# Optimization experiments

Measured on AMD Instinct MI355X. Metric: run time of the kernel, lower is better.

The kernel has to match this reference:

```python
import jax, jax.numpy as jnp
import numpy as np

N = 50000          # nodes (ogbn-products-like subgraph)
E = 800000         # directed edges (avg degree 16)
F_IN, HID, HEADS, OUT = 100, 32, 4, 47
W1 = HID * HEADS   # 128
NEG_SLOPE = 0.2
BN_EPS = 1e-5


def _gatv2(x, src, dst, w_src, w_dst, att, bias, heads, ch):
    """GATv2Conv (PyG semantics, share_weights=False, concat).
    x: [N, F]; src/dst: [Etot] (self-loops already appended);
    w_src/w_dst: [F, heads*ch]; att: [heads, ch]; bias: [heads*ch].
    """
    n = x.shape[0]
    xl = (x @ w_src).reshape(n, heads, ch)   # source-side transform
    xr = (x @ w_dst).reshape(n, heads, ch)   # target-side transform
    # per-edge attention logits: a . leaky_relu(xl[j] + xr[i])  -> [E, heads]
    e = jnp.sum(jax.nn.leaky_relu(xl[src] + xr[dst], NEG_SLOPE) * att, axis=-1)
    # segment softmax over incoming edges of each destination node
    m = jax.ops.segment_max(e, dst, num_segments=n)          # [N, heads]
    ex = jnp.exp(e - m[dst])
    denom = jax.ops.segment_sum(ex, dst, num_segments=n)     # [N, heads]
    alpha = ex / denom[dst]                                  # [E, heads]
    # weighted scatter-add aggregation of source features
    out = jax.ops.segment_sum(alpha[:, :, None] * xl[src], dst, num_segments=n)
    return out.reshape(n, heads * ch) + bias


def _bn_eval(x, g, b, m, v):
    return (x - m) * jax.lax.rsqrt(v + BN_EPS) * g + b


def setup_inputs() -> dict:
    key = jax.random.key(0)
    ks = jax.random.split(key, 32)
    s = 0.1
    inp = {
        "x": jax.random.normal(ks[0], (N, F_IN), jnp.float32),
        "edge_index": jax.random.randint(ks[1], (2, E), 0, N, dtype=jnp.int32),
        "w1_src": jax.random.normal(ks[2], (F_IN, W1), jnp.float32) * s,
        "w1_dst": jax.random.normal(ks[3], (F_IN, W1), jnp.float32) * s,
        "att1": jax.random.normal(ks[4], (HEADS, HID), jnp.float32) * s,
        "b1": jnp.zeros((W1,), jnp.float32),
        "bn1_g": jnp.ones((W1,), jnp.float32),
        "bn1_b": jnp.zeros((W1,), jnp.float32),
        "bn1_m": jax.random.normal(ks[5], (W1,), jnp.float32) * 0.05,
        "bn1_v": jax.random.uniform(ks[6], (W1,), jnp.float32, 0.5, 1.5),
        "res0_w": jax.random.normal(ks[7], (F_IN, W1), jnp.float32) * s,
        "res0_b": jnp.zeros((W1,), jnp.float32),
        "w2_src": jax.random.normal(ks[8], (W1, W1), jnp.float32) * s,
        "w2_dst": jax.random.normal(ks[9], (W1, W1), jnp.float32) * s,
        "att2": jax.random.normal(ks[10], (HEADS, HID), jnp.float32) * s,
        "b2": jnp.zeros((W1,), jnp.float32),
        "bn2_g": jnp.ones((W1,), jnp.float32),
        "bn2_b": jnp.zeros((W1,), jnp.float32),
        "bn2_m": jax.random.normal(ks[11], (W1,), jnp.float32) * 0.05,
        "bn2_v": jax.random.uniform(ks[12], (W1,), jnp.float32, 0.5, 1.5),
        # layer 3: 128 -> 47, heads=1
        "w3_src": jax.random.normal(ks[13], (W1, OUT), jnp.float32) * s,
        "w3_dst": jax.random.normal(ks[14], (W1, OUT), jnp.float32) * s,
        "att3": jax.random.normal(ks[15], (1, OUT), jnp.float32) * s,
        "b3": jnp.zeros((OUT,), jnp.float32),
        "bn3_g": jnp.ones((OUT,), jnp.float32),
        "bn3_b": jnp.zeros((OUT,), jnp.float32),
        "bn3_m": jax.random.normal(ks[16], (OUT,), jnp.float32) * 0.05,
        "bn3_v": jax.random.uniform(ks[17], (OUT,), jnp.float32, 0.5, 1.5),
        "res2_w": jax.random.normal(ks[18], (W1, OUT), jnp.float32) * s,
        "res2_b": jnp.zeros((OUT,), jnp.float32),
    }
    return inp


def reference(x, edge_index,
              w1_src, w1_dst, att1, b1, bn1_g, bn1_b, bn1_m, bn1_v, res0_w, res0_b,
              w2_src, w2_dst, att2, b2, bn2_g, bn2_b, bn2_m, bn2_v,
              w3_src, w3_dst, att3, b3, bn3_g, bn3_b, bn3_m, bn3_v, res2_w, res2_b):
    # add self-loops (PyG GATv2Conv default add_self_loops=True)
    loops = jnp.arange(x.shape[0], dtype=edge_index.dtype)
    src = jnp.concatenate([edge_index[0], loops])
    dst = jnp.concatenate([edge_index[1], loops])

    # layer 1 + linear residual + BN + relu (eval mode: no dropout)
    h = _gatv2(x, src, dst, w1_src, w1_dst, att1, b1, HEADS, HID)
    h = h + (x @ res0_w + res0_b)
    h = jax.nn.relu(_bn_eval(h, bn1_g, bn1_b, bn1_m, bn1_v))

    # layer 2 + identity residual + BN + relu
    h2 = _gatv2(h, src, dst, w2_src, w2_dst, att2, b2, HEADS, HID)
    h2 = h2 + h
    h2 = jax.nn.relu(_bn_eval(h2, bn2_g, bn2_b, bn2_m, bn2_v))

    # layer 3 (heads=1) + linear residual + BN (no relu/dropout on last layer)
    out = _gatv2(h2, src, dst, w3_src, w3_dst, att3, b3, 1, OUT)
    out = out + (h2 @ res2_w + res2_b)
    out = _bn_eval(out, bn3_g, bn3_b, bn3_m, bn3_v)
    return out
```

## Files before the change

kernel.cpp:

```cpp
#include <hip/hip_runtime.h>
#include <math.h>

#define BN_EPS 1e-5f
#define SLOT 96
#define LN16 2.7725887f

typedef _Float16 h2 __attribute__((ext_vector_type(2)));
typedef _Float16 h8 __attribute__((ext_vector_type(8)));
typedef float f2v __attribute__((ext_vector_type(2)));
typedef float float4v __attribute__((ext_vector_type(4)));

static __device__ inline h2 bit_h2(unsigned u) {
    union { unsigned u; h2 h; } c; c.u = u; return c.h;
}
static __device__ inline unsigned bit_u(h2 h) {
    union { unsigned u; h2 h; } c; c.h = h; return c.u;
}

template <int CTRL>
static __device__ inline float dpp_add(float x) {
    int y = __builtin_amdgcn_update_dpp(0, __float_as_int(x), CTRL, 0xF, 0xF, true);
    return x + __int_as_float(y);
}
static __device__ inline float red8_dpp(float t) {
    t = dpp_add<0xB1>(t); t = dpp_add<0x4E>(t); t = dpp_add<0x141>(t);
    return t;
}
static __device__ inline float red16_dpp(float t) {
    t = dpp_add<0xB1>(t); t = dpp_add<0x4E>(t); t = dpp_add<0x141>(t);
    t = dpp_add<0x140>(t);
    return t;
}

static __device__ inline void pack_one(int idx,
                                       const float* p0, const float* p1,
                                       const float* p2,
                                       int w0, int w1, int w2,
                                       int Ksrc, int Ncat,
                                       _Float16* out) {
    int k = idx / Ncat, n = idx - k * Ncat;
    float v = 0.f;
    if (k < Ksrc) {
        if (n < w0) v = p0[(size_t)k * w0 + n];
        else if (n < w0 + w1) v = p1[(size_t)k * w1 + (n - w0)];
        else if (w2 > 0 && n < w0 + w1 + w2) v = p2[(size_t)k * w2 + (n - w0 - w1)];
    }
    int kt = k >> 5, kr = k & 31;
    int quad = kr >> 3, j = kr & 7;
    int nt = n >> 4, nr = n & 15;
    int ntiles = Ncat >> 4;
    out[((size_t)(kt * ntiles + nt) * 64 + quad * 16 + nr) * 8 + j] = (_Float16)v;
}

__global__ __launch_bounds__(256) void prep_scat_k(
    const int* __restrict__ src, const int* __restrict__ dst, int E, int Etot,
    int* __restrict__ cnt, int* __restrict__ esrc, int scatBlocks,
    const float* __restrict__ x, _Float16* __restrict__ A, int N,
    const float* __restrict__ w1s, const float* __restrict__ w1d,
    const float* __restrict__ r0w, const float* __restrict__ w2s,
    const float* __restrict__ w2d, const float* __restrict__ w3s,
    const float* __restrict__ w3d, const float* __restrict__ r2w,
    _Float16* __restrict__ Wb1, _Float16* __restrict__ Wb2,
    _Float16* __restrict__ Wb3) {
    if ((int)blockIdx.x < scatBlocks) {
        int i = blockIdx.x * 256 + threadIdx.x;
        if (i < Etot) {
            int d = (i < E) ? dst[i] : (i - E);
            int s = (i < E) ? src[i] : (i - E);
            int pos = atomicAdd(&cnt[d], 1);
            esrc[(size_t)d * SLOT + pos] = s << 9;
        }
        return;
    }
    const int S1 = 128 * 384, S2 = 128 * 256, S3 = 128 * 144;
    int convTot = N * 128;
    int idx = (blockIdx.x - scatBlocks) * 256 + threadIdx.x;
    if (idx < convTot) {
        int n = idx >> 7, k = idx & 127;
        A[idx] = (_Float16)(k < 100 ? x[(size_t)n * 100 + k] : 0.f);
        return;
    }
    int p = idx - convTot;
    if (p < S1) pack_one(p, w1s, w1d, r0w, 128, 128, 128, 100, 384, Wb1);
    else if (p < S1 + S2) pack_one(p - S1, w2s, w2d, nullptr, 128, 128, 0, 128, 256, Wb2);
    else if (p < S1 + S2 + S3) pack_one(p - S1 - S2, w3s, w3d, r2w, 47, 47, 47, 128, 144, Wb3);
}

template <int NT>
__global__ __launch_bounds__(256) void mfma_gemm(const _Float16* __restrict__ A,
                                                 const _Float16* __restrict__ Bp,
                                                 _Float16* __restrict__ XLR,
                                                 float* __restrict__ RES,
                                                 int M, int Kpad, int Ncat,
                                                 int ncat_valid, int res_off,
                                                 int bf_remap, int bf_shift,
                                                 int bf_stride, int res_stride) {
    int wid = (blockIdx.x * 256 + threadIdx.x) >> 6;
    int lane = threadIdx.x & 63;
    int ngroups = Ncat / (16 * NT);
    int mtiles = M >> 4;
    int mt = wid / ngroups;
    int ng = wid - mt * ngroups;
    if (mt >= mtiles) return;
    int quad = lane >> 4;
    int nr = lane & 15;
    int row = mt * 16 + nr;
    int ntiles = Ncat >> 4;

    float4v acc[NT];
#pragma unroll
    for (int t = 0; t < NT; t++) acc[t] = (float4v){0.f, 0.f, 0.f, 0.f};

    for (int k0 = 0; k0 < Kpad; k0 += 32) {
        h8 a = *(const h8*)(A + (size_t)row * Kpad + k0 + quad * 8);
        int kt = k0 >> 5;
        const _Float16* bbase =
            Bp + ((size_t)(kt * ntiles + ng * NT) * 64 + lane) * 8;
#pragma unroll
        for (int t = 0; t < NT; t++) {
            h8 b = *(const h8*)(bbase + (size_t)t * 64 * 8);
            acc[t] = __builtin_amdgcn_mfma_f32_16x16x32_f16(a, b, acc[t], 0, 0, 0);
        }
    }
    int rowb = mt * 16 + quad * 4;
#pragma unroll
    for (int t = 0; t < NT; t++) {
        int col = (ng * NT + t) * 16 + nr;
        if (col >= ncat_valid) continue;
        if (col < res_off) {
            int bc = (col >= bf_remap) ? col + bf_shift : col;
#pragma unroll
            for (int r = 0; r < 4; r++)
                XLR[(size_t)(rowb + r) * bf_stride + bc] = (_Float16)acc[t][r];
        } else {
            int rc = col - res_off;
#pragma unroll
            for (int r = 0; r < 4; r++)
                RES[(size_t)(rowb + r) * res_stride + rc] = acc[t][r];
        }
    }
}

__global__ __launch_bounds__(256) void gat_agg4_fused(
    const int* __restrict__ cnt, const int* __restrict__ esrc,
    const _Float16* __restrict__ xlr, const float* __restrict__ att,
    const float* __restrict__ RES, const float* __restrict__ resB,
    const float* __restrict__ bias,
    const float* __restrict__ g, const float* __restrict__ bb,
    const float* __restrict__ mm, const float* __restrict__ vv,
    _Float16* __restrict__ hbf, int N, int mode) {
    int d = blockIdx.x * 4 + (threadIdx.x >> 6);
    if (d >= N) return;
    int lane = threadIdx.x & 63;
    int half = lane >> 5;
    int gl = lane & 31;
    int c0 = gl * 4;
    const char* xb = (const char*)xlr + c0 * 2;
    const h2 NS = {(_Float16)0.2f, (_Float16)0.2f};

    uint2 xrv = *(const uint2*)(xb + (size_t)d * 512 + 256);
    h2 xr01 = bit_h2(xrv.x), xr23 = bit_h2(xrv.y);
    float4 af = *(const float4*)(att + c0);
    h2 at01 = {(_Float16)af.x, (_Float16)af.y};
    h2 at23 = {(_Float16)af.z, (_Float16)af.w};

    int beg = d * SLOT;
    int end = beg + cnt[d];
    float den = 0.f;
    h2 acc01 = {(_Float16)0.f, (_Float16)0.f};
    h2 acc23 = acc01;
    int j = beg;
    for (; j + 4 <= end; j += 4) {
        int o0 = esrc[j + half];
        int o1 = esrc[j + 2 + half];
        uint2 u0 = *(const uint2*)(xb + o0);
        uint2 u1 = *(const uint2*)(xb + o1);
        h2 a01 = bit_h2(u0.x), a23 = bit_h2(u0.y);
        h2 b01 = bit_h2(u1.x), b23 = bit_h2(u1.y);
        h2 v01 = a01 + xr01, v23 = a23 + xr23;
        h2 w01 = b01 + xr01, w23 = b23 + xr23;
        v01 = __builtin_elementwise_max(v01, v01 * NS);
        v23 = __builtin_elementwise_max(v23, v23 * NS);
        w01 = __builtin_elementwise_max(w01, w01 * NS);
        w23 = __builtin_elementwise_max(w23, w23 * NS);
        h2 t2a = v01 * at01 + v23 * at23;
        h2 t2b = w01 * at01 + w23 * at23;
        f2v ta = __builtin_convertvector(t2a, f2v);
        f2v tb = __builtin_convertvector(t2b, f2v);
        float t0 = ta.x + ta.y;
        float t1 = tb.x + tb.y;
        t0 = red8_dpp(t0);
        t1 = red8_dpp(t1);
        float p0 = __expf(t0 - LN16);
        float p1 = __expf(t1 - LN16);
        den += p0 + p1;
        h2 P0 = {(_Float16)p0, (_Float16)p0};
        h2 P1 = {(_Float16)p1, (_Float16)p1};
        acc01 = P0 * a01 + acc01;
        acc23 = P0 * a23 + acc23;
        acc01 = P1 * b01 + acc01;
        acc23 = P1 * b23 + acc23;
    }
    for (; j < end; j += 2) {
        int jj = j + half;
        bool act = jj < end;
        int o = esrc[act ? jj : (end - 1)];
        uint2 u0 = *(const uint2*)(xb + o);
        h2 a01 = bit_h2(u0.x), a23 = bit_h2(u0.y);
        h2 v01 = a01 + xr01, v23 = a23 + xr23;
        v01 = __builtin_elementwise_max(v01, v01 * NS);
        v23 = __builtin_elementwise_max(v23, v23 * NS);
        h2 t2 = v01 * at01 + v23 * at23;
        f2v tf = __builtin_convertvector(t2, f2v);
        float t = tf.x + tf.y;
        t = red8_dpp(t);
        float p = act ? __expf(t - LN16) : 0.f;
        den += p;
        h2 P = {(_Float16)p, (_Float16)p};
        acc01 = P * a01 + acc01;
        acc23 = P * a23 + acc23;
    }
    den += __shfl_xor(den, 32);
    f2v c01 = __builtin_convertvector(acc01, f2v);
    f2v c23 = __builtin_convertvector(acc23, f2v);
    float f0 = c01.x, f1 = c01.y, fA = c23.x, fB = c23.y;
    f0 += __shfl_xor(f0, 32);
    f1 += __shfl_xor(f1, 32);
    fA += __shfl_xor(fA, 32);
    fB += __shfl_xor(fB, 32);

    if (half == 0) {
        float inv = 1.f / den;
        float4 bi = *(const float4*)(bias + c0);
        float o0 = f0 * inv + bi.x;
        float o1 = f1 * inv + bi.y;
        float o2 = fA * inv + bi.z;
        float o3 = fB * inv + bi.w;
        if (mode == 1) {
            float4 r = *(const float4*)(RES + (size_t)d * 128 + c0);
            float4 rb = *(const float4*)(resB + c0);
            o0 += r.x + rb.x; o1 += r.y + rb.y;
            o2 += r.z + rb.z; o3 += r.w + rb.w;
        } else {
            uint2 hv = *(const uint2*)(hbf + (size_t)d * 128 + c0);
            f2v g01 = __builtin_convertvector(bit_h2(hv.x), f2v);
            f2v g23 = __builtin_convertvector(bit_h2(hv.y), f2v);
            o0 += g01.x; o1 += g01.y; o2 += g23.x; o3 += g23.y;
        }
        float4 gm = *(const float4*)(mm + c0);
        float4 gv = *(const float4*)(vv + c0);
        float4 gg = *(const float4*)(g + c0);
        float4 gb = *(const float4*)(bb + c0);
        o0 = fmaxf((o0 - gm.x) * rsqrtf(gv.x + BN_EPS) * gg.x + gb.x, 0.f);
        o1 = fmaxf((o1 - gm.y) * rsqrtf(gv.y + BN_EPS) * gg.y + gb.y, 0.f);
        o2 = fmaxf((o2 - gm.z) * rsqrtf(gv.z + BN_EPS) * gg.z + gb.z, 0.f);
        o3 = fmaxf((o3 - gm.w) * rsqrtf(gv.w + BN_EPS) * gg.w + gb.w, 0.f);
        h2 s01 = {(_Float16)o0, (_Float16)o1};
        h2 s23 = {(_Float16)o2, (_Float16)o3};
        uint2 w;
        w.x = bit_u(s01);
        w.y = bit_u(s23);
        *(uint2*)(hbf + (size_t)d * 128 + c0) = w;
    }
}

__global__ __launch_bounds__(256) void gat_agg1_fused(
    const int* __restrict__ cnt, const int* __restrict__ esrc,
    const _Float16* __restrict__ xlr, const float* __restrict__ att,
    const float* __restrict__ RES, const float* __restrict__ resB,
    const float* __restrict__ bias,
    const float* __restrict__ g, const float* __restrict__ bb,
    const float* __restrict__ mm, const float* __restrict__ vv,
    float* __restrict__ out, int N) {
    int d = blockIdx.x * 4 + (threadIdx.x >> 6);
    if (d >= N) return;
    int lane = threadIdx.x & 63;
    int gl = lane & 15, grp = lane >> 4;
    const char* xb = (const char*)xlr + gl * 8;
    const h2 NS = {(_Float16)0.2f, (_Float16)0.2f};

    uint2 xrv = *(const uint2*)(xb + (size_t)d * 256 + 128);
    h2 xr01 = bit_h2(xrv.x), xr23 = bit_h2(xrv.y);
    float atf[4];
#pragma unroll
    for (int k = 0; k < 4; k++) {
        int c = gl * 4 + k;
        atf[k] = (c < 47) ? att[c] : 0.f;
    }
    h2 at01 = {(_Float16)atf[0], (_Float16)atf[1]};
    h2 at23 = {(_Float16)atf[2], (_Float16)atf[3]};

    int beg = d * SLOT;
    int end = beg + cnt[d];
    float den = 0.f;
    h2 acc01 = {(_Float16)0.f, (_Float16)0.f};
    h2 acc23 = acc01;
    int j = beg + grp;
    for (; j + 4 < end; j += 8) {
        int o0 = esrc[j] >> 1;
        int o1 = esrc[j + 4] >> 1;
        uint2 u0 = *(const uint2*)(xb + o0);
        uint2 u1 = *(const uint2*)(xb + o1);
        h2 a01 = bit_h2(u0.x), a23 = bit_h2(u0.y);
        h2 b01 = bit_h2(u1.x), b23 = bit_h2(u1.y);
        h2 v01 = a01 + xr01, v23 = a23 + xr23;
        h2 w01 = b01 + xr01, w23 = b23 + xr23;
        v01 = __builtin_elementwise_max(v01, v01 * NS);
        v23 = __builtin_elementwise_max(v23, v23 * NS);
        w01 = __builtin_elementwise_max(w01, w01 * NS);
        w23 = __builtin_elementwise_max(w23, w23 * NS);
        h2 t2a = v01 * at01 + v23 * at23;
        h2 t2b = w01 * at01 + w23 * at23;
        f2v ta = __builtin_convertvector(t2a, f2v);
        f2v tb = __builtin_convertvector(t2b, f2v);
        float t0 = ta.x + ta.y;
        float t1 = tb.x + tb.y;
        t0 = red16_dpp(t0);
        t1 = red16_dpp(t1);
        float p0 = __expf(t0 - LN16);
        float p1 = __expf(t1 - LN16);
        den += p0 + p1;
        h2 P0 = {(_Float16)p0, (_Float16)p0};
        h2 P1 = {(_Float16)p1, (_Float16)p1};
        acc01 = P0 * a01 + acc01;
        acc23 = P0 * a23 + acc23;
        acc01 = P1 * b01 + acc01;
        acc23 = P1 * b23 + acc23;
    }
    if (j < end) {
        int o = esrc[j] >> 1;
        uint2 u0 = *(const uint2*)(xb + o);
        h2 a01 = bit_h2(u0.x), a23 = bit_h2(u0.y);
        h2 v01 = a01 + xr01, v23 = a23 + xr23;
        v01 = __builtin_elementwise_max(v01, v01 * NS);
        v23 = __builtin_elementwise_max(v23, v23 * NS);
        h2 t2 = v01 * at01 + v23 * at23;
        f2v tf = __builtin_convertvector(t2, f2v);
        float t = tf.x + tf.y;
        t = red16_dpp(t);
        float p = __expf(t - LN16);
        den += p;
        h2 P = {(_Float16)p, (_Float16)p};
        acc01 = P * a01 + acc01;
        acc23 = P * a23 + acc23;
    }
    den += __shfl_xor(den, 16);
    den += __shfl_xor(den, 32);
    f2v c01 = __builtin_convertvector(acc01, f2v);
    f2v c23 = __builtin_convertvector(acc23, f2v);
    float f[4] = {c01.x, c01.y, c23.x, c23.y};
#pragma unroll
    for (int k = 0; k < 4; k++) {
        f[k] += __shfl_xor(f[k], 16);
        f[k] += __shfl_xor(f[k], 32);
    }
    if (grp == 0 && gl < 12) {
        float inv = 1.f / den;
#pragma unroll
        for (int k = 0; k < 4; k++) {
            int c = gl * 4 + k;
            if (c < 47) {
                float o = f[k] * inv + bias[c] + RES[(size_t)d * 48 + c] + resB[c];
                o = (o - mm[c]) * rsqrtf(vv[c] + BN_EPS) * g[c] + bb[c];
                out[(size_t)d * 47 + c] = o;
            }
        }
    }
}

extern "C" void kernel_launch(void* const* d_in, const int* in_sizes, int n_in,
                              void* d_out, int out_size, void* d_ws, size_t ws_size,
                              hipStream_t stream) {
    const float* x      = (const float*)d_in[0];
    const int*   ei     = (const int*)d_in[1];
    const float* w1_src = (const float*)d_in[2];
    const float* w1_dst = (const float*)d_in[3];
    const float* att1   = (const float*)d_in[4];
    const float* b1     = (const float*)d_in[5];
    const float* bn1_g  = (const float*)d_in[6];
    const float* bn1_b  = (const float*)d_in[7];
    const float* bn1_m  = (const float*)d_in[8];
    const float* bn1_v  = (const float*)d_in[9];
    const float* res0_w = (const float*)d_in[10];
    const float* res0_b = (const float*)d_in[11];
    const float* w2_src = (const float*)d_in[12];
    const float* w2_dst = (const float*)d_in[13];
    const float* att2   = (const float*)d_in[14];
    const float* b2     = (const float*)d_in[15];
    const float* bn2_g  = (const float*)d_in[16];
    const float* bn2_b  = (const float*)d_in[17];
    const float* bn2_m  = (const float*)d_in[18];
    const float* bn2_v  = (const float*)d_in[19];
    const float* w3_src = (const float*)d_in[20];
    const float* w3_dst = (const float*)d_in[21];
    const float* att3   = (const float*)d_in[22];
    const float* b3     = (const float*)d_in[23];
    const float* bn3_g  = (const float*)d_in[24];
    const float* bn3_b  = (const float*)d_in[25];
    const float* bn3_m  = (const float*)d_in[26];
    const float* bn3_v  = (const float*)d_in[27];
    const float* res2_w = (const float*)d_in[28];
    const float* res2_b = (const float*)d_in[29];

    const int F_IN = 100;
    const int KP = 128;
    const int NC1 = 384, NC2 = 256, NC3 = 144;
    int N = in_sizes[0] / F_IN;
    int E = in_sizes[1] / 2;
    int Etot = E + N;
    const int* src = ei;
    const int* dst = ei + E;

    float* ws = (float*)d_ws;
    size_t o = 0;
    _Float16* XLR = (_Float16*)(ws + o); o += (size_t)N * 128;
    float* B_res = ws + o; o += (size_t)N * 128;
    _Float16* A_h = (_Float16*)(ws + o); o += (size_t)N * 64;
    _Float16* Wb1 = (_Float16*)(ws + o); o += (size_t)KP * NC1 / 2;
    _Float16* Wb2 = (_Float16*)(ws + o); o += (size_t)KP * NC2 / 2;
    _Float16* Wb3 = (_Float16*)(ws + o); o += (size_t)KP * NC3 / 2;
    int* I_cnt  = (int*)(ws + o); o += N;
    int* I_esrc = (int*)(ws + o); o += (size_t)N * SLOT + 4;
    (void)ws_size; (void)n_in; (void)out_size;

    int mtiles = (N + 15) / 16;
    int aggGrid = (N + 3) / 4;

    hipMemsetAsync(I_cnt, 0, (size_t)N * sizeof(int), stream);

    {
        int sb = (Etot + 255) / 256;
        int prepTot = N * KP + KP * (NC1 + NC2 + NC3);
        int pb = (prepTot + 255) / 256;
        prep_scat_k<<<sb + pb, 256, 0, stream>>>(
            src, dst, E, Etot, I_cnt, I_esrc, sb, x, A_h, N,
            w1_src, w1_dst, res0_w, w2_src, w2_dst, w3_src, w3_dst, res2_w,
            Wb1, Wb2, Wb3);
    }

    {
        int waves = mtiles * (NC1 / 64);
        mfma_gemm<4><<<(waves + 3) / 4, 256, 0, stream>>>(
            A_h, Wb1, XLR, B_res, N, KP, NC1, 384, 256, 384, 0, 256, 128);
    }
    gat_agg4_fused<<<aggGrid, 256, 0, stream>>>(
        I_cnt, I_esrc, XLR, att1, B_res, res0_b, b1,
        bn1_g, bn1_b, bn1_m, bn1_v, A_h, N, 1);

    {
        int waves = mtiles * (NC2 / 64);
        mfma_gemm<4><<<(waves + 3) / 4, 256, 0, stream>>>(
            A_h, Wb2, XLR, B_res, N, KP, NC2, 256, 256, 256, 0, 256, 128);
    }
    gat_agg4_fused<<<aggGrid, 256, 0, stream>>>(
        I_cnt, I_esrc, XLR, att2, nullptr, nullptr, b2,
        bn2_g, bn2_b, bn2_m, bn2_v, A_h, N, 2);

    {
        int waves = mtiles * (NC3 / 48);
        mfma_gemm<3><<<(waves + 3) / 4, 256, 0, stream>>>(
            A_h, Wb3, XLR, B_res, N, KP, NC3, 141, 94, 47, 17, 128, 48);
    }
    gat_agg1_fused<<<aggGrid, 256, 0, stream>>>(
        I_cnt, I_esrc, XLR, att3, B_res, res2_b, b3,
        bn3_g, bn3_b, bn3_m, bn3_v, (float*)d_out, N);
}
```

Baseline: 394.4 us.

## Fuse all stages into one persistent cooperative kernel with grid syncs

Replaces the memset and seven separate kernel launches with a single cooperative persistent kernel. Stages are separated by grid.sync() and use grid-stride loops. The edge scatter now overlaps with the first GEMM, and per-thread BN constants are hoisted out of the node loop. The aim is to remove launch gaps and tail effects, at the cost of grid-wide barrier overhead and occupancy capped by the fused kernel's register use.

```diff
diff --git a/kernel.cpp b/kernel.cpp
--- a/kernel.cpp
+++ b/kernel.cpp
@@ -1,5 +1,8 @@
 #include <hip/hip_runtime.h>
+#include <hip/hip_cooperative_groups.h>
 #include <math.h>
+
+namespace cg = cooperative_groups;
 
 #define BN_EPS 1e-5f
 #define SLOT 96
@@ -31,6 +34,24 @@
     t = dpp_add<0x140>(t);
     return t;
 }
+
+struct P {
+    const int* src; const int* dst; int E; int Etot; int N;
+    const float* x;
+    const float* w1s; const float* w1d; const float* r0w; const float* r0b;
+    const float* att1; const float* b1;
+    const float* bn1g; const float* bn1b; const float* bn1m; const float* bn1v;
+    const float* w2s; const float* w2d;
+    const float* att2; const float* b2;
+    const float* bn2g; const float* bn2b; const float* bn2m; const float* bn2v;
+    const float* w3s; const float* w3d; const float* r2w; const float* r2b;
+    const float* att3; const float* b3;
+    const float* bn3g; const float* bn3b; const float* bn3m; const float* bn3v;
+    _Float16* XLR; float* RES; _Float16* A;
+    _Float16* Wb1; _Float16* Wb2; _Float16* Wb3;
+    int* cnt; int* esrc;
+    float* out;
+};
 
 static __device__ inline void pack_one(int idx,
                                        const float* p0, const float* p1,
@@ -52,364 +73,342 @@
     out[((size_t)(kt * ntiles + nt) * 64 + quad * 16 + nr) * 8 + j] = (_Float16)v;
 }
 
-__global__ __launch_bounds__(256) void prep_scat_k(
-    const int* __restrict__ src, const int* __restrict__ dst, int E, int Etot,
-    int* __restrict__ cnt, int* __restrict__ esrc, int scatBlocks,
-    const float* __restrict__ x, _Float16* __restrict__ A, int N,
-    const float* __restrict__ w1s, const float* __restrict__ w1d,
-    const float* __restrict__ r0w, const float* __restrict__ w2s,
-    const float* __restrict__ w2d, const float* __restrict__ w3s,
-    const float* __restrict__ w3d, const float* __restrict__ r2w,
-    _Float16* __restrict__ Wb1, _Float16* __restrict__ Wb2,
-    _Float16* __restrict__ Wb3) {
-    if ((int)blockIdx.x < scatBlocks) {
-        int i = blockIdx.x * 256 + threadIdx.x;
-        if (i < Etot) {
-            int d = (i < E) ? dst[i] : (i - E);
-            int s = (i < E) ? src[i] : (i - E);
-            int pos = atomicAdd(&cnt[d], 1);
-            esrc[(size_t)d * SLOT + pos] = s << 9;
-        }
-        return;
-    }
-    const int S1 = 128 * 384, S2 = 128 * 256, S3 = 128 * 144;
-    int convTot = N * 128;
-    int idx = (blockIdx.x - scatBlocks) * 256 + threadIdx.x;
-    if (idx < convTot) {
-        int n = idx >> 7, k = idx & 127;
-        A[idx] = (_Float16)(k < 100 ? x[(size_t)n * 100 + k] : 0.f);
-        return;
-    }
-    int p = idx - convTot;
-    if (p < S1) pack_one(p, w1s, w1d, r0w, 128, 128, 128, 100, 384, Wb1);
-    else if (p < S1 + S2) pack_one(p - S1, w2s, w2d, nullptr, 128, 128, 0, 128, 256, Wb2);
-    else if (p < S1 + S2 + S3) pack_one(p - S1 - S2, w3s, w3d, r2w, 47, 47, 47, 128, 144, Wb3);
-}
-
 template <int NT>
-__global__ __launch_bounds__(256) void mfma_gemm(const _Float16* __restrict__ A,
-                                                 const _Float16* __restrict__ Bp,
-                                                 _Float16* __restrict__ XLR,
-                                                 float* __restrict__ RES,
-                                                 int M, int Kpad, int Ncat,
-                                                 int ncat_valid, int res_off,
-                                                 int bf_remap, int bf_shift,
-                                                 int bf_stride, int res_stride) {
-    int wid = (blockIdx.x * 256 + threadIdx.x) >> 6;
+static __device__ void gemm_phase(const _Float16* __restrict__ A,
+                                  const _Float16* __restrict__ Bp,
+                                  _Float16* __restrict__ XLR,
+                                  float* __restrict__ RES,
+                                  int M, int Ncat, int ncat_valid, int res_off,
+                                  int bf_remap, int bf_shift,
+                                  int bf_stride, int res_stride) {
     int lane = threadIdx.x & 63;
+    int gw = blockIdx.x * 4 + (threadIdx.x >> 6);
+    int gws = gridDim.x * 4;
     int ngroups = Ncat / (16 * NT);
     int mtiles = M >> 4;
-    int mt = wid / ngroups;
-    int ng = wid - mt * ngroups;
-    if (mt >= mtiles) return;
+    int ntiles = Ncat >> 4;
     int quad = lane >> 4;
     int nr = lane & 15;
-    int row = mt * 16 + nr;
-    int ntiles = Ncat >> 4;
-
-    float4v acc[NT];
-#pragma unroll
-    for (int t = 0; t < NT; t++) acc[t] = (float4v){0.f, 0.f, 0.f, 0.f};
-
-    for (int k0 = 0; k0 < Kpad; k0 += 32) {
-        h8 a = *(const h8*)(A + (size_t)row * Kpad + k0 + quad * 8);
-        int kt = k0 >> 5;
-        const _Float16* bbase =
-            Bp + ((size_t)(kt * ntiles + ng * NT) * 64 + lane) * 8;
+    for (int w = gw; w < mtiles * ngroups; w += gws) {
+        int mt = w / ngroups;
+        int ng = w - mt * ngroups;
+        int row = mt * 16 + nr;
+        float4v acc[NT];
+#pragma unroll
+        for (int t = 0; t < NT; t++) acc[t] = (float4v){0.f, 0.f, 0.f, 0.f};
+#pragma unroll
+        for (int k0 = 0; k0 < 128; k0 += 32) {
+            h8 a = *(const h8*)(A + (size_t)row * 128 + k0 + quad * 8);
+            int kt = k0 >> 5;
+            const _Float16* bbase =
+                Bp + ((size_t)(kt * ntiles + ng * NT) * 64 + lane) * 8;
+#pragma unroll
+            for (int t = 0; t < NT; t++) {
+                h8 b = *(const h8*)(bbase + (size_t)t * 512);
+                acc[t] = __builtin_amdgcn_mfma_f32_16x16x32_f16(a, b, acc[t], 0, 0, 0);
+            }
+        }
+        int rowb = mt * 16 + quad * 4;
 #pragma unroll
         for (int t = 0; t < NT; t++) {
-            h8 b = *(const h8*)(bbase + (size_t)t * 64 * 8);
-            acc[t] = __builtin_amdgcn_mfma_f32_16x16x32_f16(a, b, acc[t], 0, 0, 0);
-        }
-    }
-    int rowb = mt * 16 + quad * 4;
-#pragma unroll
-    for (int t = 0; t < NT; t++) {
-        int col = (ng * NT + t) * 16 + nr;
-        if (col >= ncat_valid) continue;
-        if (col < res_off) {
-            int bc = (col >= bf_remap) ? col + bf_shift : col;
-#pragma unroll
-            for (int r = 0; r < 4; r++)
-                XLR[(size_t)(rowb + r) * bf_stride + bc] = (_Float16)acc[t][r];
-        } else {
-            int rc = col - res_off;
-#pragma unroll
-            for (int r = 0; r < 4; r++)
-                RES[(size_t)(rowb + r) * res_stride + rc] = acc[t][r];
-        }
-    }
-}
-
-__global__ __launch_bounds__(256) void gat_agg4_fused(
-    const int* __restrict__ cnt, const int* __restrict__ esrc,
-    const _Float16* __restrict__ xlr, const float* __restrict__ att,
-    const float* __restrict__ RES, const float* __restrict__ resB,
-    const float* __restrict__ bias,
-    const float* __restrict__ g, const float* __restrict__ bb,
-    const float* __restrict__ mm, const float* __restrict__ vv,
-    _Float16* __restrict__ hbf, int N, int mode) {
-    int d = blockIdx.x * 4 + (threadIdx.x >> 6);
-    if (d >= N) return;
+            int col = (ng * NT + t) * 16 + nr;
+            if (col >= ncat_valid) continue;
+            if (col < res_off) {
+                int bc = (col >= bf_remap) ? col + bf_shift : col;
+#pragma unroll
+                for (int r = 0; r < 4; r++)
+                    XLR[(size_t)(rowb + r) * bf_stride + bc] = (_Float16)acc[t][r];
+            } else {
+                int rc = col - res_off;
+#pragma unroll
+                for (int r = 0; r < 4; r++)
+                    RES[(size_t)(rowb + r) * res_stride + rc] = acc[t][r];
+            }
+        }
+    }
+}
+
+static __device__ void agg4_phase(const P& p, const float* __restrict__ att,
+                                  const float* __restrict__ RES,
+                                  const float* __restrict__ resB,
+                                  const float* __restrict__ bias,
+                                  const float* __restrict__ g,
+                                  const float* __restrict__ bb,
+                                  const float* __restrict__ mm,
+                                  const float* __restrict__ vv, int mode) {
+    int gw = blockIdx.x * 4 + (threadIdx.x >> 6);
+    int gws = gridDim.x * 4;
     int lane = threadIdx.x & 63;
     int half = lane >> 5;
     int gl = lane & 31;
     int c0 = gl * 4;
-    const char* xb = (const char*)xlr + c0 * 2;
+    const char* xb = (const char*)p.XLR + c0 * 2;
     const h2 NS = {(_Float16)0.2f, (_Float16)0.2f};
 
-    uint2 xrv = *(const uint2*)(xb + (size_t)d * 512 + 256);
-    h2 xr01 = bit_h2(xrv.x), xr23 = bit_h2(xrv.y);
     float4 af = *(const float4*)(att + c0);
     h2 at01 = {(_Float16)af.x, (_Float16)af.y};
     h2 at23 = {(_Float16)af.z, (_Float16)af.w};
-
-    int beg = d * SLOT;
-    int end = beg + cnt[d];
-    float den = 0.f;
-    h2 acc01 = {(_Float16)0.f, (_Float16)0.f};
-    h2 acc23 = acc01;
-    int j = beg;
-    for (; j + 4 <= end; j += 4) {
-        int o0 = esrc[j + half];
-        int o1 = esrc[j + 2 + half];
-        uint2 u0 = *(const uint2*)(xb + o0);
-        uint2 u1 = *(const uint2*)(xb + o1);
-        h2 a01 = bit_h2(u0.x), a23 = bit_h2(u0.y);
-        h2 b01 = bit_h2(u1.x), b23 = bit_h2(u1.y);
-        h2 v01 = a01 + xr01, v23 = a23 + xr23;
-        h2 w01 = b01 + xr01, w23 = b23 + xr23;
-        v01 = __builtin_elementwise_max(v01, v01 * NS);
-        v23 = __builtin_elementwise_max(v23, v23 * NS);
-        w01 = __builtin_elementwise_max(w01, w01 * NS);
-        w23 = __builtin_elementwise_max(w23, w23 * NS);
-        h2 t2a = v01 * at01 + v23 * at23;
-        h2 t2b = w01 * at01 + w23 * at23;
-        f2v ta = __builtin_convertvector(t2a, f2v);
-        f2v tb = __builtin_convertvector(t2b, f2v);
-        float t0 = ta.x + ta.y;
-        float t1 = tb.x + tb.y;
-        t0 = red8_dpp(t0);
-        t1 = red8_dpp(t1);
-        float p0 = __expf(t0 - LN16);
-        float p1 = __expf(t1 - LN16);
-        den += p0 + p1;
-        h2 P0 = {(_Float16)p0, (_Float16)p0};
-        h2 P1 = {(_Float16)p1, (_Float16)p1};
-        acc01 = P0 * a01 + acc01;
-        acc23 = P0 * a23 + acc23;
-        acc01 = P1 * b01 + acc01;
-        acc23 = P1 * b23 + acc23;
-    }
-    for (; j < end; j += 2) {
-        int jj = j + half;
-        bool act = jj < end;
-        int o = esrc[act ? jj : (end - 1)];
-        uint2 u0 = *(const uint2*)(xb + o);
-        h2 a01 = bit_h2(u0.x), a23 = bit_h2(u0.y);
-        h2 v01 = a01 + xr01, v23 = a23 + xr23;
-        v01 = __builtin_elementwise_max(v01, v01 * NS);
-        v23 = __builtin_elementwise_max(v23, v23 * NS);
-        h2 t2 = v01 * at01 + v23 * at23;
-        f2v tf = __builtin_convertvector(t2, f2v);
-        float t = tf.x + tf.y;
-        t = red8_dpp(t);
-        float p = act ? __expf(t - LN16) : 0.f;
-        den += p;
-        h2 P = {(_Float16)p, (_Float16)p};
-        acc01 = P * a01 + acc01;
-        acc23 = P * a23 + acc23;
-    }
-    den += __shfl_xor(den, 32);
-    f2v c01 = __builtin_convertvector(acc01, f2v);
-    f2v c23 = __builtin_convertvector(acc23, f2v);
-    float f0 = c01.x, f1 = c01.y, fA = c23.x, fB = c23.y;
-    f0 += __shfl_xor(f0, 32);
-    f1 += __shfl_xor(f1, 32);
-    fA += __shfl_xor(fA, 32);
-    fB += __shfl_xor(fB, 32);
-
-    if (half == 0) {
-        float inv = 1.f / den;
-        float4 bi = *(const float4*)(bias + c0);
-        float o0 = f0 * inv + bi.x;
-        float o1 = f1 * inv + bi.y;
-        float o2 = fA * inv + bi.z;
-        float o3 = fB * inv + bi.w;
-        if (mode == 1) {
-            float4 r = *(const float4*)(RES + (size_t)d * 128 + c0);
-            float4 rb = *(const float4*)(resB + c0);
-            o0 += r.x + rb.x; o1 += r.y + rb.y;
-            o2 += r.z + rb.z; o3 += r.w + rb.w;
-        } else {
-            uint2 hv = *(const uint2*)(hbf + (size_t)d * 128 + c0);
-            f2v g01 = __builtin_convertvector(bit_h2(hv.x), f2v);
-            f2v g23 = __builtin_convertvector(bit_h2(hv.y), f2v);
-            o0 += g01.x; o1 += g01.y; o2 += g23.x; o3 += g23.y;
-        }
-        float4 gm = *(const float4*)(mm + c0);
-        float4 gv = *(const float4*)(vv + c0);
-        float4 gg = *(const float4*)(g + c0);
-        float4 gb = *(const float4*)(bb + c0);
-        o0 = fmaxf((o0 - gm.x) * rsqrtf(gv.x + BN_EPS) * gg.x + gb.x, 0.f);
-        o1 = fmaxf((o1 - gm.y) * rsqrtf(gv.y + BN_EPS) * gg.y + gb.y, 0.f);
-        o2 = fmaxf((o2 - gm.z) * rsqrtf(gv.z + BN_EPS) * gg.z + gb.z, 0.f);
-        o3 = fmaxf((o3 - gm.w) * rsqrtf(gv.w + BN_EPS) * gg.w + gb.w, 0.f);
-        h2 s01 = {(_Float16)o0, (_Float16)o1};
-        h2 s23 = {(_Float16)o2, (_Float16)o3};
-        uint2 w;
-        w.x = bit_u(s01);
-        w.y = bit_u(s23);
-        *(uint2*)(hbf + (size_t)d * 128 + c0) = w;
-    }
-}
-
-__global__ __launch_bounds__(256) void gat_agg1_fused(
-    const int* __restrict__ cnt, const int* __restrict__ esrc,
-    const _Float16* __restrict__ xlr, const float* __restrict__ att,
-    const float* __restrict__ RES, const float* __restrict__ resB,
-    const float* __restrict__ bias,
-    const float* __restrict__ g, const float* __restrict__ bb,
-    const float* __restrict__ mm, const float* __restrict__ vv,
-    float* __restrict__ out, int N) {
-    int d = blockIdx.x * 4 + (threadIdx.x >> 6);
-    if (d >= N) return;
+    float4 bi = *(const float4*)(bias + c0);
+    float4 gm = *(const float4*)(mm + c0);
+    float4 gv = *(const float4*)(vv + c0);
+    float4 gg = *(const float4*)(g + c0);
+    float4 gb = *(const float4*)(bb + c0);
+    float4 rb = (mode == 1) ? *(const float4*)(resB + c0)
+                            : (float4){0.f, 0.f, 0.f, 0.f};
+    float rs0 = rsqrtf(gv.x + BN_EPS), rs1 = rsqrtf(gv.y + BN_EPS);
+    float rs2 = rsqrtf(gv.z + BN_EPS), rs3 = rsqrtf(gv.w + BN_EPS);
+
+    for (int d = gw; d < p.N; d += gws) {
+        uint2 xrv = *(const uint2*)(xb + (size_t)d * 512 + 256);
+        h2 xr01 = bit_h2(xrv.x), xr23 = bit_h2(xrv.y);
+        int beg = d * SLOT;
+        int end = beg + p.cnt[d];
+        float den = 0.f;
+        h2 acc01 = {(_Float16)0.f, (_Float16)0.f};
+        h2 acc23 = acc01;
+        int j = beg;
+        for (; j + 4 <= end; j += 4) {
+            int o0 = p.esrc[j + half];
+            int o1 = p.esrc[j + 2 + half];
+            uint2 u0 = *(const uint2*)(xb + o0);
+            uint2 u1 = *(const uint2*)(xb + o1);
+            h2 a01 = bit_h2(u0.x), a23 = bit_h2(u0.y);
+            h2 b01 = bit_h2(u1.x), b23 = bit_h2(u1.y);
+            h2 v01 = a01 + xr01, v23 = a23 + xr23;
+            h2 w01 = b01 + xr01, w23 = b23 + xr23;
+            v01 = __builtin_elementwise_max(v01, v01 * NS);
+            v23 = __builtin_elementwise_max(v23, v23 * NS);
+            w01 = __builtin_elementwise_max(w01, w01 * NS);
+            w23 = __builtin_elementwise_max(w23, w23 * NS);
+            h2 t2a = v01 * at01 + v23 * at23;
+            h2 t2b = w01 * at01 + w23 * at23;
+            f2v ta = __builtin_convertvector(t2a, f2v);
+            f2v tb = __builtin_convertvector(t2b, f2v);
+            float t0 = red8_dpp(ta.x + ta.y);
+            float t1 = red8_dpp(tb.x + tb.y);
+            float p0 = __expf(t0 - LN16);
+            float p1 = __expf(t1 - LN16);
+            den += p0 + p1;
+            h2 P0 = {(_Float16)p0, (_Float16)p0};
+            h2 P1 = {(_Float16)p1, (_Float16)p1};
+            acc01 = P0 * a01 + acc01;
+            acc23 = P0 * a23 + acc23;
+            acc01 = P1 * b01 + acc01;
+            acc23 = P1 * b23 + acc23;
+        }
+        for (; j < end; j += 2) {
+            int jj = j + half;
+            bool act = jj < end;
+            int o = p.esrc[act ? jj : (end - 1)];
+            uint2 u0 = *(const uint2*)(xb + o);
+            h2 a01 = bit_h2(u0.x), a23 = bit_h2(u0.y);
+            h2 v01 = a01 + xr01, v23 = a23 + xr23;
+            v01 = __builtin_elementwise_max(v01, v01 * NS);
+            v23 = __builtin_elementwise_max(v23, v23 * NS);
+            h2 t2 = v01 * at01 + v23 * at23;
+            f2v tf = __builtin_convertvector(t2, f2v);
+            float t = red8_dpp(tf.x + tf.y);
+            float pp = act ? __expf(t - LN16) : 0.f;
+            den += pp;
+            h2 PP = {(_Float16)pp, (_Float16)pp};
+            acc01 = PP * a01 + acc01;
+            acc23 = PP * a23 + acc23;
+        }
+        den += __shfl_xor(den, 32);
+        f2v c01 = __builtin_convertvector(acc01, f2v);
+        f2v c23 = __builtin_convertvector(acc23, f2v);
+        float f0 = c01.x, f1 = c01.y, fA = c23.x, fB = c23.y;
+        f0 += __shfl_xor(f0, 32);
+        f1 += __shfl_xor(f1, 32);
+        fA += __shfl_xor(fA, 32);
+        fB += __shfl_xor(fB, 32);
+
+        if (half == 0) {
+            float inv = 1.f / den;
+            float o0 = f0 * inv + bi.x;
+            float o1 = f1 * inv + bi.y;
+            float o2 = fA * inv + bi.z;
+            float o3 = fB * inv + bi.w;
+            if (mode == 1) {
+                float4 r = *(const float4*)(RES + (size_t)d * 128 + c0);
+                o0 += r.x + rb.x; o1 += r.y + rb.y;
+                o2 += r.z + rb.z; o3 += r.w + rb.w;
+            } else {
+                uint2 hv = *(const uint2*)(p.A + (size_t)d * 128 + c0);
+                f2v g01 = __builtin_convertvector(bit_h2(hv.x), f2v);
+                f2v g23 = __builtin_convertvector(bit_h2(hv.y), f2v);
+                o0 += g01.x; o1 += g01.y; o2 += g23.x; o3 += g23.y;
+            }
+            o0 = fmaxf((o0 - gm.x) * rs0 * gg.x + gb.x, 0.f);
+            o1 = fmaxf((o1 - gm.y) * rs1 * gg.y + gb.y, 0.f);
+            o2 = fmaxf((o2 - gm.z) * rs2 * gg.z + gb.z, 0.f);
+            o3 = fmaxf((o3 - gm.w) * rs3 * gg.w + gb.w, 0.f);
+            h2 s01 = {(_Float16)o0, (_Float16)o1};
+            h2 s23 = {(_Float16)o2, (_Float16)o3};
+            uint2 w;
+            w.x = bit_u(s01);
+            w.y = bit_u(s23);
+            *(uint2*)(p.A + (size_t)d * 128 + c0) = w;
+        }
+    }
+}
+
+static __device__ void agg1_phase(const P& p) {
+    int gw = blockIdx.x * 4 + (threadIdx.x >> 6);
+    int gws = gridDim.x * 4;
     int lane = threadIdx.x & 63;
     int gl = lane & 15, grp = lane >> 4;
-    const char* xb = (const char*)xlr + gl * 8;
+    const char* xb = (const char*)p.XLR + gl * 8;
     const h2 NS = {(_Float16)0.2f, (_Float16)0.2f};
 
-    uint2 xrv = *(const uint2*)(xb + (size_t)d * 256 + 128);
-    h2 xr01 = bit_h2(xrv.x), xr23 = bit_h2(xrv.y);
     float atf[4];
 #pragma unroll
     for (int k = 0; k < 4; k++) {
         int c = gl * 4 + k;
-        atf[k] = (c < 47) ? att[c] : 0.f;
+        atf[k] = (c < 47) ? p.att3[c] : 0.f;
     }
     h2 at01 = {(_Float16)atf[0], (_Float16)atf[1]};
     h2 at23 = {(_Float16)atf[2], (_Float16)atf[3]};
 
-    int beg = d * SLOT;
-    int end = beg + cnt[d];
-    float den = 0.f;
-    h2 acc01 = {(_Float16)0.f, (_Float16)0.f};
-    h2 acc23 = acc01;
-    int j = beg + grp;
-    for (; j + 4 < end; j += 8) {
-        int o0 = esrc[j] >> 1;
-        int o1 = esrc[j + 4] >> 1;
-        uint2 u0 = *(const uint2*)(xb + o0);
-        uint2 u1 = *(const uint2*)(xb + o1);
-        h2 a01 = bit_h2(u0.x), a23 = bit_h2(u0.y);
-        h2 b01 = bit_h2(u1.x), b23 = bit_h2(u1.y);
-        h2 v01 = a01 + xr01, v23 = a23 + xr23;
-        h2 w01 = b01 + xr01, w23 = b23 + xr23;
-        v01 = __builtin_elementwise_max(v01, v01 * NS);
-        v23 = __builtin_elementwise_max(v23, v23 * NS);
-        w01 = __builtin_elementwise_max(w01, w01 * NS);
-        w23 = __builtin_elementwise_max(w23, w23 * NS);
-        h2 t2a = v01 * at01 + v23 * at23;
-        h2 t2b = w01 * at01 + w23 * at23;
-        f2v ta = __builtin_convertvector(t2a, f2v);
-        f2v tb = __builtin_convertvector(t2b, f2v);
-        float t0 = ta.x + ta.y;
-        float t1 = tb.x + tb.y;
-        t0 = red16_dpp(t0);
-        t1 = red16_dpp(t1);
-        float p0 = __expf(t0 - LN16);
-        float p1 = __expf(t1 - LN16);
-        den += p0 + p1;
-        h2 P0 = {(_Float16)p0, (_Float16)p0};
-        h2 P1 = {(_Float16)p1, (_Float16)p1};
-        acc01 = P0 * a01 + acc01;
-        acc23 = P0 * a23 + acc23;
-        acc01 = P1 * b01 + acc01;
-        acc23 = P1 * b23 + acc23;
-    }
-    if (j < end) {
-        int o = esrc[j] >> 1;
-        uint2 u0 = *(const uint2*)(xb + o);
-        h2 a01 = bit_h2(u0.x), a23 = bit_h2(u0.y);
-        h2 v01 = a01 + xr01, v23 = a23 + xr23;
-        v01 = __builtin_elementwise_max(v01, v01 * NS);
-        v23 = __builtin_elementwise_max(v23, v23 * NS);
-        h2 t2 = v01 * at01 + v23 * at23;
-        f2v tf = __builtin_convertvector(t2, f2v);
-        float t = tf.x + tf.y;
-        t = red16_dpp(t);
-        float p = __expf(t - LN16);
-        den += p;
-        h2 P = {(_Float16)p, (_Float16)p};
-        acc01 = P * a01 + acc01;
-        acc23 = P * a23 + acc23;
-    }
-    den += __shfl_xor(den, 16);
-    den += __shfl_xor(den, 32);
-    f2v c01 = __builtin_convertvector(acc01, f2v);
-    f2v c23 = __builtin_convertvector(acc23, f2v);
-    float f[4] = {c01.x, c01.y, c23.x, c23.y};
-#pragma unroll
-    for (int k = 0; k < 4; k++) {
-        f[k] += __shfl_xor(f[k], 16);
-        f[k] += __shfl_xor(f[k], 32);
-    }
-    if (grp == 0 && gl < 12) {
-        float inv = 1.f / den;
+    for (int d = gw; d < p.N; d += gws) {
+        uint2 xrv = *(const uint2*)(xb + (size_t)d * 256 + 128);
+        h2 xr01 = bit_h2(xrv.x), xr23 = bit_h2(xrv.y);
+        int beg = d * SLOT;
+        int end = beg + p.cnt[d];
+        float den = 0.f;
+        h2 acc01 = {(_Float16)0.f, (_Float16)0.f};
+        h2 acc23 = acc01;
+        int j = beg + grp;
+        for (; j + 4 < end; j += 8) {
+            int o0 = p.esrc[j] >> 1;
+            int o1 = p.esrc[j + 4] >> 1;
+            uint2 u0 = *(const uint2*)(xb + o0);
+            uint2 u1 = *(const uint2*)(xb + o1);
+            h2 a01 = bit_h2(u0.x), a23 = bit_h2(u0.y);
+            h2 b01 = bit_h2(u1.x), b23 = bit_h2(u1.y);
+            h2 v01 = a01 + xr01, v23 = a23 + xr23;
+            h2 w01 = b01 + xr01, w23 = b23 + xr23;
+            v01 = __builtin_elementwise_max(v01, v01 * NS);
+            v23 = __builtin_elementwise_max(v23, v23 * NS);
+            w01 = __builtin_elementwise_max(w01, w01 * NS);
+            w23 = __builtin_elementwise_max(w23, w23 * NS);
+            h2 t2a = v01 * at01 + v23 * at23;
+            h2 t2b = w01 * at01 + w23 * at23;
+            f2v ta = __builtin_convertvector(t2a, f2v);
+            f2v tb = __builtin_convertvector(t2b, f2v);
+            float t0 = red16_dpp(ta.x + ta.y);
+            float t1 = red16_dpp(tb.x + tb.y);
+            float p0 = __expf(t0 - LN16);
+            float p1 = __expf(t1 - LN16);
+            den += p0 + p1;
+            h2 P0 = {(_Float16)p0, (_Float16)p0};
+            h2 P1 = {(_Float16)p1, (_Float16)p1};
+            acc01 = P0 * a01 + acc01;
+            acc23 = P0 * a23 + acc23;
+            acc01 = P1 * b01 + acc01;
+            acc23 = P1 * b23 + acc23;
+        }
+        if (j < end) {
+            int o = p.esrc[j] >> 1;
+            uint2 u0 = *(const uint2*)(xb + o);
+            h2 a01 = bit_h2(u0.x), a23 = bit_h2(u0.y);
+            h2 v01 = a01 + xr01, v23 = a23 + xr23;
+            v01 = __builtin_elementwise_max(v01, v01 * NS);
+            v23 = __builtin_elementwise_max(v23, v23 * NS);
+            h2 t2 = v01 * at01 + v23 * at23;
+            f2v tf = __builtin_convertvector(t2, f2v);
+            float t = red16_dpp(tf.x + tf.y);
+            float pp = __expf(t - LN16);
+            den += pp;
+            h2 PP = {(_Float16)pp, (_Float16)pp};
+            acc01 = PP * a01 + acc01;
+            acc23 = PP * a23 + acc23;
+        }
+        den += __shfl_xor(den, 16);
+        den += __shfl_xor(den, 32);
+        f2v c01 = __builtin_convertvector(acc01, f2v);
+        f2v c23 = __builtin_convertvector(acc23, f2v);
+        float f[4] = {c01.x, c01.y, c23.x, c23.y};
 #pragma unroll
         for (int k = 0; k < 4; k++) {
-            int c = gl * 4 + k;
-            if (c < 47) {
-                float o = f[k] * inv + bias[c] + RES[(size_t)d * 48 + c] + resB[c];
-                o = (o - mm[c]) * rsqrtf(vv[c] + BN_EPS) * g[c] + bb[c];
-                out[(size_t)d * 47 + c] = o;
+            f[k] += __shfl_xor(f[k], 16);
+            f[k] += __shfl_xor(f[k], 32);
+        }
+        if (grp == 0 && gl < 12) {
+            float inv = 1.f / den;
+#pragma unroll
+            for (int k = 0; k < 4; k++) {
+                int c = gl * 4 + k;
+                if (c < 47) {
+                    float o = f[k] * inv + p.b3[c] + p.RES[(size_t)d * 48 + c]
+                              + p.r2b[c];
+                    o = (o - p.bn3m[c]) * rsqrtf(p.bn3v[c] + BN_EPS) * p.bn3g[c]
+                        + p.bn3b[c];
+                    p.out[(size_t)d * 47 + c] = o;
+                }
             }
         }
     }
+}
+
+__global__ __launch_bounds__(256, 4) void fused_k(P p) {
+    cg::grid_group grid = cg::this_grid();
+    int tid = blockIdx.x * 256 + threadIdx.x;
+    int gs = gridDim.x * 256;
+
+    {
+        const int S1 = 128 * 384, S2 = 128 * 256, S3 = 128 * 144;
+        int convTot = p.N * 128;
+        int tot = p.N + convTot + S1 + S2 + S3;
+        for (int i = tid; i < tot; i += gs) {
+            if (i < p.N) {
+                p.cnt[i] = 0;
+            } else if (i < p.N + convTot) {
+                int idx = i - p.N;
+                int n = idx >> 7, k = idx & 127;
+                p.A[idx] = (_Float16)(k < 100 ? p.x[(size_t)n * 100 + k] : 0.f);
+            } else {
+                int q = i - p.N - convTot;
+                if (q < S1) pack_one(q, p.w1s, p.w1d, p.r0w, 128, 128, 128, 100, 384, p.Wb1);
+                else if (q < S1 + S2) pack_one(q - S1, p.w2s, p.w2d, nullptr, 128, 128, 0, 128, 256, p.Wb2);
+                else pack_one(q - S1 - S2, p.w3s, p.w3d, p.r2w, 47, 47, 47, 128, 144, p.Wb3);
+            }
+        }
+    }
+    grid.sync();
+
+    for (int i = tid; i < p.Etot; i += gs) {
+        int d = (i < p.E) ? p.dst[i] : (i - p.E);
+        int s = (i < p.E) ? p.src[i] : (i - p.E);
+        int pos = atomicAdd(&p.cnt[d], 1);
+        p.esrc[(size_t)d * SLOT + pos] = s << 9;
+    }
+    gemm_phase<4>(p.A, p.Wb1, p.XLR, p.RES, p.N, 384, 384, 256, 384, 0, 256, 128);
+    grid.sync();
+
+    agg4_phase(p, p.att1, p.RES, p.r0b, p.b1, p.bn1g, p.bn1b, p.bn1m, p.bn1v, 1);
+    grid.sync();
+
+    gemm_phase<4>(p.A, p.Wb2, p.XLR, p.RES, p.N, 256, 256, 256, 256, 0, 256, 128);
+    grid.sync();
+
+    agg4_phase(p, p.att2, nullptr, nullptr, p.b2, p.bn2g, p.bn2b, p.bn2m, p.bn2v, 2);
+    grid.sync();
+
+    gemm_phase<3>(p.A, p.Wb3, p.XLR, p.RES, p.N, 144, 141, 94, 47, 17, 128, 48);
+    grid.sync();
+
+    agg1_phase(p);
 }
 
 extern "C" void kernel_launch(void* const* d_in, const int* in_sizes, int n_in,
                               void* d_out, int out_size, void* d_ws, size_t ws_size,
                               hipStream_t stream) {
-    const float* x      = (const float*)d_in[0];
-    const int*   ei     = (const int*)d_in[1];
-    const float* w1_src = (const float*)d_in[2];
-    const float* w1_dst = (const float*)d_in[3];
-    const float* att1   = (const float*)d_in[4];
-    const float* b1     = (const float*)d_in[5];
-    const float* bn1_g  = (const float*)d_in[6];
-    const float* bn1_b  = (const float*)d_in[7];
-    const float* bn1_m  = (const float*)d_in[8];
-    const float* bn1_v  = (const float*)d_in[9];
-    const float* res0_w = (const float*)d_in[10];
-    const float* res0_b = (const float*)d_in[11];
-    const float* w2_src = (const float*)d_in[12];
-    const float* w2_dst = (const float*)d_in[13];
-    const float* att2   = (const float*)d_in[14];
-    const float* b2     = (const float*)d_in[15];
-    const float* bn2_g  = (const float*)d_in[16];
-    const float* bn2_b  = (const float*)d_in[17];
-    const float* bn2_m  = (const float*)d_in[18];
-    const float* bn2_v  = (const float*)d_in[19];
-    const float* w3_src = (const float*)d_in[20];
-    const float* w3_dst = (const float*)d_in[21];
-    const float* att3   = (const float*)d_in[22];
-    const float* b3     = (const float*)d_in[23];
-    const float* bn3_g  = (const float*)d_in[24];
-    const float* bn3_b  = (const float*)d_in[25];
-    const float* bn3_m  = (const float*)d_in[26];
-    const float* bn3_v  = (const float*)d_in[27];
-    const float* res2_w = (const float*)d_in[28];
-    const float* res2_b = (const float*)d_in[29];
-
     const int F_IN = 100;
     const int KP = 128;
     const int NC1 = 384, NC2 = 256, NC3 = 144;
     int N = in_sizes[0] / F_IN;
     int E = in_sizes[1] / 2;
-    int Etot = E + N;
-    const int* src = ei;
-    const int* dst = ei + E;
 
     float* ws = (float*)d_ws;
     size_t o = 0;
@@ -423,45 +422,38 @@
     int* I_esrc = (int*)(ws + o); o += (size_t)N * SLOT + 4;
     (void)ws_size; (void)n_in; (void)out_size;
 
-    int mtiles = (N + 15) / 16;
-    int aggGrid = (N + 3) / 4;
-
-    hipMemsetAsync(I_cnt, 0, (size_t)N * sizeof(int), stream);
-
-    {
-        int sb = (Etot + 255) / 256;
-        int prepTot = N * KP + KP * (NC1 + NC2 + NC3);
-        int pb = (prepTot + 255) / 256;
-        prep_scat_k<<<sb + pb, 256, 0, stream>>>(
-            src, dst, E, Etot, I_cnt, I_esrc, sb, x, A_h, N,
-            w1_src, w1_dst, res0_w, w2_src, w2_dst, w3_src, w3_dst, res2_w,
-            Wb1, Wb2, Wb3);
-    }
-
-    {
-        int waves = mtiles * (NC1 / 64);
-        mfma_gemm<4><<<(waves + 3) / 4, 256, 0, stream>>>(
-            A_h, Wb1, XLR, B_res, N, KP, NC1, 384, 256, 384, 0, 256, 128);
-    }
-    gat_agg4_fused<<<aggGrid, 256, 0, stream>>>(
-        I_cnt, I_esrc, XLR, att1, B_res, res0_b, b1,
-        bn1_g, bn1_b, bn1_m, bn1_v, A_h, N, 1);
-
-    {
-        int waves = mtiles * (NC2 / 64);
-        mfma_gemm<4><<<(waves + 3) / 4, 256, 0, stream>>>(
-            A_h, Wb2, XLR, B_res, N, KP, NC2, 256, 256, 256, 0, 256, 128);
-    }
-    gat_agg4_fused<<<aggGrid, 256, 0, stream>>>(
-        I_cnt, I_esrc, XLR, att2, nullptr, nullptr, b2,
-        bn2_g, bn2_b, bn2_m, bn2_v, A_h, N, 2);
-
-    {
-        int waves = mtiles * (NC3 / 48);
-        mfma_gemm<3><<<(waves + 3) / 4, 256, 0, stream>>>(
-            A_h, Wb3, XLR, B_res, N, KP, NC3, 141, 94, 47, 17, 128, 48);
-    }
-    gat_agg1_fused<<<aggGrid, 256, 0, stream>>>(
-        I_cnt, I_esrc, XLR, att3, B_res, res2_b, b3,
-        bn3_g, bn3_b, bn3_m, bn3_v, (float*)d_out, N);
-}
+    P p;
+    p.src = (const int*)d_in[1];
+    p.dst = (const int*)d_in[1] + E;
+    p.E = E; p.Etot = E + N; p.N = N;
+    p.x = (const float*)d_in[0];
+    p.w1s = (const float*)d_in[2];  p.w1d = (const float*)d_in[3];
+    p.att1 = (const float*)d_in[4]; p.b1 = (const float*)d_in[5];
+    p.bn1g = (const float*)d_in[6]; p.bn1b = (const float*)d_in[7];
+    p.bn1m = (const float*)d_in[8]; p.bn1v = (const float*)d_in[9];
+    p.r0w = (const float*)d_in[10]; p.r0b = (const float*)d_in[11];
+    p.w2s = (const float*)d_in[12]; p.w2d = (const float*)d_in[13];
+    p.att2 = (const float*)d_in[14]; p.b2 = (const float*)d_in[15];
+    p.bn2g = (const float*)d_in[16]; p.bn2b = (const float*)d_in[17];
+    p.bn2m = (const float*)d_in[18]; p.bn2v = (const float*)d_in[19];
+    p.w3s = (const float*)d_in[20]; p.w3d = (const float*)d_in[21];
+    p.att3 = (const float*)d_in[22]; p.b3 = (const float*)d_in[23];
+    p.bn3g = (const float*)d_in[24]; p.bn3b = (const float*)d_in[25];
+    p.bn3m = (const float*)d_in[26]; p.bn3v = (const float*)d_in[27];
+    p.r2w = (const float*)d_in[28]; p.r2b = (const float*)d_in[29];
+    p.XLR = XLR; p.RES = B_res; p.A = A_h;
+    p.Wb1 = Wb1; p.Wb2 = Wb2; p.Wb3 = Wb3;
+    p.cnt = I_cnt; p.esrc = I_esrc;
+    p.out = (float*)d_out;
+
+    int perCU = 0;
+    hipError_t qerr = hipOccupancyMaxActiveBlocksPerMultiprocessor(
+        &perCU, (const void*)fused_k, 256, 0);
+    if (qerr != hipSuccess || perCU < 1) perCU = 1;
+    if (perCU > 4) perCU = 4;
+    int nblk = perCU * 256;
+
+    void* args[] = { (void*)&p };
+    hipLaunchCooperativeKernel((void*)fused_k, dim3(nblk), dim3(256), args, 0,
+                               stream);
+}
```

Result: slower. 1.092 ms (+176.9%).
